# Performance work log

Hardware: AMD Instinct MI355X
Metric: run time of the kernel (lower is better)

## Reference

```python
import jax, jax.numpy as jnp
import numpy as np

KH = KW = 3
PAD = 1
STRIDE = 1
C_IN = 32
C_OUT = 16
H = W = 64
B = 64
H_OUT = (H - KH + 2 * PAD) // STRIDE + 1
W_OUT = (W - KW + 2 * PAD) // STRIDE + 1
S = H_OUT * W_OUT
K = C_IN * KH * KW


def unfold_2d(x):
    # x: [B, C, H, W] -> [B, C*KH*KW, S], torch.nn.functional.unfold ordering
    xp = jnp.pad(x, ((0, 0), (0, 0), (PAD, PAD), (PAD, PAD)))
    patches = []
    for i in range(KH):
        for j in range(KW):
            patches.append(xp[:, :, i:i + H_OUT * STRIDE:STRIDE, j:j + W_OUT * STRIDE:STRIDE])
    u = jnp.stack(patches, axis=2)  # [B, C, KH*KW, H_OUT, W_OUT]
    return u.reshape(x.shape[0], K, S)


def setup_inputs() -> dict:
    key = jax.random.key(0)
    k1, k2, k3 = jax.random.split(key, 3)
    X = jax.random.normal(k1, (B, C_IN, H, W), dtype=jnp.float32)
    # kaiming normal (linear): std = 1/sqrt(fan_in), fan_in = K for each location's GEMM
    weight = jax.random.normal(k2, (S, K, C_OUT), dtype=jnp.float32) / jnp.sqrt(jnp.float32(K))
    # xavier uniform over [H_OUT, W_OUT]
    lim = np.sqrt(6.0 / (H_OUT + W_OUT))
    bias = jax.random.uniform(k3, (H_OUT, W_OUT), dtype=jnp.float32, minval=-lim, maxval=lim)
    return {"X": X, "weight": weight, "bias": bias}


def reference(X, weight, bias):
    ufld = unfold_2d(X)                               # [B, K, S]
    ufld = ufld + bias.reshape(1, 1, -1)              # bias added per-location to patches
    h = jnp.einsum('bks,skc->bcs', ufld, weight)      # per-location unshared GEMM
    return h.reshape(X.shape[0], C_OUT, H_OUT, W_OUT)
```

## Files before the change

### kernel.cpp

```cpp
#include <hip/hip_runtime.h>
#include <stdint.h>
#include <stddef.h>

#define HOUT 64
#define WOUT 64
#define CIN  32
#define COUT 16
#define BATCH 64
#define SLOC 4096
#define KTOT 288
#define HPAD 66

typedef __attribute__((ext_vector_type(8))) short  short8;
typedef __attribute__((ext_vector_type(4))) float  floatx4;

static __device__ __forceinline__ unsigned short f2bf(float f) {
    union { float f; unsigned int u; } v; v.f = f;
    unsigned int u = v.u;
    unsigned int r = (u + 0x7FFFu + ((u >> 16) & 1u)) >> 16;
    return (unsigned short)r;
}

__global__ __launch_bounds__(256, 4) void prep_kernel(const float* __restrict__ X,
                                                      const float* __restrict__ Wg,
                                                      const float* __restrict__ bias,
                                                      unsigned short* __restrict__ xt,
                                                      uint4* __restrict__ wt,
                                                      float* __restrict__ bsum) {
    const int id   = blockIdx.x;
    const int tid  = threadIdx.x;
    const int lane = tid & 63;
    const int wv   = tid >> 6;

    if (id < 260) {
        int h1, w1;
        if (id < 66)       { h1 = 0;  w1 = id; }
        else if (id < 132) { h1 = 65; w1 = id - 66; }
        else { int r = id - 132; h1 = (r >> 1) + 1; w1 = (r & 1) ? 65 : 0; }
        ((uint4*)(xt + (size_t)(h1 * HPAD + w1) * 2048))[tid] = uint4{0u, 0u, 0u, 0u};
    }

    {
        const int w   = tid >> 2;
        const int cg8 = (tid & 3) * 8;
#pragma unroll
        for (int u = 0; u < 4; ++u) {
            const int unit = id * 4 + u;
            const int h = unit >> 6, b = unit & 63;
            const float* xb = X + (((size_t)b * CIN + cg8) * HOUT + h) * WOUT + w;
            unsigned short v[8];
#pragma unroll
            for (int j = 0; j < 8; ++j)
                v[j] = f2bf(xb[(size_t)j * HOUT * WOUT]);
            uint4 pack;
            pack.x = (unsigned)v[0] | ((unsigned)v[1] << 16);
            pack.y = (unsigned)v[2] | ((unsigned)v[3] << 16);
            pack.z = (unsigned)v[4] | ((unsigned)v[5] << 16);
            pack.w = (unsigned)v[6] | ((unsigned)v[7] << 16);
            *(uint4*)(xt + (size_t)((h + 1) * HPAD + (w + 1)) * 2048 + b * CIN + cg8) = pack;
        }
    }

    {
        const int lo = id & 7;
        const int q4 = (id >> 3) & 3;
        const int g  = ((id >> 5) << 3) | lo;
        const int s  = g * 16 + q4 * 4 + wv;
        const int q = lane >> 4, n = lane & 15;

        const float* wb = Wg + (size_t)s * (KTOT * COUT) + (size_t)(8 * q) * 9 * COUT + n;
        float csum = 0.f;
#pragma unroll
        for (int t = 0; t < 9; ++t) {
            float w[8];
#pragma unroll
            for (int j = 0; j < 8; ++j)
                w[j] = wb[(size_t)t * COUT + (size_t)j * 9 * COUT];
            unsigned short hh[8];
#pragma unroll
            for (int j = 0; j < 8; ++j) { csum += w[j]; hh[j] = f2bf(w[j]); }
            uint4 pack;
            pack.x = (unsigned)hh[0] | ((unsigned)hh[1] << 16);
            pack.y = (unsigned)hh[2] | ((unsigned)hh[3] << 16);
            pack.z = (unsigned)hh[4] | ((unsigned)hh[5] << 16);
            pack.w = (unsigned)hh[6] | ((unsigned)hh[7] << 16);
            wt[(size_t)(s * 9 + t) * 64 + lane] = pack;
        }
        csum += __shfl_xor(csum, 16, 64);
        csum += __shfl_xor(csum, 32, 64);
        if (lane < 16) bsum[s * COUT + n] = bias[s] * csum;
    }
}

__global__ __launch_bounds__(256, 4) void varconv_kernel(const unsigned short* __restrict__ xt,
                                                         const uint4* __restrict__ wt,
                                                         const float* __restrict__ bsum,
                                                         float* __restrict__ out) {
    __shared__ float lds[16 * 324];

    int id = blockIdx.x;
    int lo = id & 7;
    int q4 = (id >> 3) & 3;
    int g  = ((id >> 5) << 3) | lo;
    int s0 = g * 16;
    int y  = s0 >> 6;
    int x0 = s0 & 63;
    int B0 = q4 * 16;

    int lane = threadIdx.x & 63, wv = threadIdx.x >> 6;
    int q = lane >> 4;
    int n = lane & 15;

#pragma unroll
    for (int i = 0; i < 4; ++i) {
        int sl = wv * 4 + i;
        int s  = s0 + sl;
        int x  = x0 + sl;

        const uint4* wf = wt + (size_t)s * 9 * 64 + lane;
        short8 bf[9];
#pragma unroll
        for (int t = 0; t < 9; ++t)
            bf[t] = *(const short8*)(wf + t * 64);

        float badd = bsum[s * COUT + n];

        const unsigned short* ab = xt + (size_t)(B0 + n) * CIN + q * 8;
        short8 af[9];
#pragma unroll
        for (int t = 0; t < 9; ++t) {
            const int cy = t / 3, cx = t % 3;
            af[t] = *(const short8*)(ab + (size_t)((y + cy) * HPAD + (x + cx)) * 2048);
        }

        floatx4 acc = {0.f, 0.f, 0.f, 0.f};
#pragma unroll
        for (int t = 0; t < 9; ++t)
            acc = __builtin_amdgcn_mfma_f32_16x16x32_bf16(af[t], bf[t], acc, 0, 0, 0);

        int slot = q ^ (n & 3);
        floatx4 v = {acc[0] + badd, acc[1] + badd, acc[2] + badd, acc[3] + badd};
        *(floatx4*)&lds[n * 324 + sl * 20 + slot * 4] = v;
    }

    __syncthreads();

    int c   = lane >> 2;
    int slg = lane & 3;
#pragma unroll
    for (int i2 = 0; i2 < 4; ++i2) {
        int ib   = wv * 4 + i2;
        int slot = (ib >> 2) ^ (c & 3);
        float o0[4];
#pragma unroll
        for (int e = 0; e < 4; ++e)
            o0[e] = lds[c * 324 + (slg * 4 + e) * 20 + slot * 4 + (ib & 3)];
        floatx4 o = {o0[0], o0[1], o0[2], o0[3]};
        *(floatx4*)(out + ((size_t)((B0 + ib) * COUT + c)) * SLOC + s0 + slg * 4) = o;
    }
}

extern "C" void kernel_launch(void* const* d_in, const int* in_sizes, int n_in,
                              void* d_out, int out_size, void* d_ws, size_t ws_size,
                              hipStream_t stream) {
    const float* X    = (const float*)d_in[0];
    const float* Wg   = (const float*)d_in[1];
    const float* bias = (const float*)d_in[2];
    float* out = (float*)d_out;

    unsigned short* xt = (unsigned short*)d_ws;
    uint4* wt   = (uint4*)((char*)d_ws + 17842176);
    float* bsum = (float*)((char*)d_ws + 17842176 + 37748736);

    prep_kernel<<<1024, 256, 0, stream>>>(X, Wg, bias, xt, wt, bsum);
    varconv_kernel<<<1024, 256, 0, stream>>>(xt, wt, bsum, out);
}
```

Baseline: 166.0 us.

## Fuse weight bf16 conversion and bias-sum into conv kernel, drop workspace round-trip

Weight conversion to bf16 and the per-location weight column sums used for the bias term now happen inside the conv kernel, read straight from the fp32 weights. This removes writing and re-reading a ~38MB bf16 weight buffer and the bsum buffer through global memory. The prep kernel now only transposes X, split over twice as many blocks with half the work each. The trade-off is that the conv kernel does strided fp32 weight loads and extra conversion work per wave, which can raise register pressure.

```diff
diff --git a/kernel.cpp b/kernel.cpp
--- a/kernel.cpp
+++ b/kernel.cpp
@@ -21,16 +21,10 @@
     return (unsigned short)r;
 }
 
-__global__ __launch_bounds__(256, 4) void prep_kernel(const float* __restrict__ X,
-                                                      const float* __restrict__ Wg,
-                                                      const float* __restrict__ bias,
-                                                      unsigned short* __restrict__ xt,
-                                                      uint4* __restrict__ wt,
-                                                      float* __restrict__ bsum) {
-    const int id   = blockIdx.x;
-    const int tid  = threadIdx.x;
-    const int lane = tid & 63;
-    const int wv   = tid >> 6;
+__global__ __launch_bounds__(256) void prep_kernel(const float* __restrict__ X,
+                                                   unsigned short* __restrict__ xt) {
+    const int id  = blockIdx.x;
+    const int tid = threadIdx.x;
 
     if (id < 260) {
         int h1, w1;
@@ -40,61 +34,29 @@
         ((uint4*)(xt + (size_t)(h1 * HPAD + w1) * 2048))[tid] = uint4{0u, 0u, 0u, 0u};
     }
 
-    {
-        const int w   = tid >> 2;
-        const int cg8 = (tid & 3) * 8;
+    const int w   = tid >> 2;
+    const int cg8 = (tid & 3) * 8;
 #pragma unroll
-        for (int u = 0; u < 4; ++u) {
-            const int unit = id * 4 + u;
-            const int h = unit >> 6, b = unit & 63;
-            const float* xb = X + (((size_t)b * CIN + cg8) * HOUT + h) * WOUT + w;
-            unsigned short v[8];
+    for (int u = 0; u < 2; ++u) {
+        const int unit = id * 2 + u;
+        const int h = unit >> 6, b = unit & 63;
+        const float* xb = X + (((size_t)b * CIN + cg8) * HOUT + h) * WOUT + w;
+        unsigned short v[8];
 #pragma unroll
-            for (int j = 0; j < 8; ++j)
-                v[j] = f2bf(xb[(size_t)j * HOUT * WOUT]);
-            uint4 pack;
-            pack.x = (unsigned)v[0] | ((unsigned)v[1] << 16);
-            pack.y = (unsigned)v[2] | ((unsigned)v[3] << 16);
-            pack.z = (unsigned)v[4] | ((unsigned)v[5] << 16);
-            pack.w = (unsigned)v[6] | ((unsigned)v[7] << 16);
-            *(uint4*)(xt + (size_t)((h + 1) * HPAD + (w + 1)) * 2048 + b * CIN + cg8) = pack;
-        }
-    }
-
-    {
-        const int lo = id & 7;
-        const int q4 = (id >> 3) & 3;
-        const int g  = ((id >> 5) << 3) | lo;
-        const int s  = g * 16 + q4 * 4 + wv;
-        const int q = lane >> 4, n = lane & 15;
-
-        const float* wb = Wg + (size_t)s * (KTOT * COUT) + (size_t)(8 * q) * 9 * COUT + n;
-        float csum = 0.f;
-#pragma unroll
-        for (int t = 0; t < 9; ++t) {
-            float w[8];
-#pragma unroll
-            for (int j = 0; j < 8; ++j)
-                w[j] = wb[(size_t)t * COUT + (size_t)j * 9 * COUT];
-            unsigned short hh[8];
-#pragma unroll
-            for (int j = 0; j < 8; ++j) { csum += w[j]; hh[j] = f2bf(w[j]); }
-            uint4 pack;
-            pack.x = (unsigned)hh[0] | ((unsigned)hh[1] << 16);
-            pack.y = (unsigned)hh[2] | ((unsigned)hh[3] << 16);
-            pack.z = (unsigned)hh[4] | ((unsigned)hh[5] << 16);
-            pack.w = (unsigned)hh[6] | ((unsigned)hh[7] << 16);
-            wt[(size_t)(s * 9 + t) * 64 + lane] = pack;
-        }
-        csum += __shfl_xor(csum, 16, 64);
-        csum += __shfl_xor(csum, 32, 64);
-        if (lane < 16) bsum[s * COUT + n] = bias[s] * csum;
+        for (int j = 0; j < 8; ++j)
+            v[j] = f2bf(xb[(size_t)j * HOUT * WOUT]);
+        uint4 pack;
+        pack.x = (unsigned)v[0] | ((unsigned)v[1] << 16);
+        pack.y = (unsigned)v[2] | ((unsigned)v[3] << 16);
+        pack.z = (unsigned)v[4] | ((unsigned)v[5] << 16);
+        pack.w = (unsigned)v[6] | ((unsigned)v[7] << 16);
+        *(uint4*)(xt + (size_t)((h + 1) * HPAD + (w + 1)) * 2048 + b * CIN + cg8) = pack;
     }
 }
 
 __global__ __launch_bounds__(256, 4) void varconv_kernel(const unsigned short* __restrict__ xt,
-                                                         const uint4* __restrict__ wt,
-                                                         const float* __restrict__ bsum,
+                                                         const float* __restrict__ Wg,
+                                                         const float* __restrict__ bias,
                                                          float* __restrict__ out) {
     __shared__ float lds[16 * 324];
 
@@ -117,14 +79,6 @@
         int s  = s0 + sl;
         int x  = x0 + sl;
 
-        const uint4* wf = wt + (size_t)s * 9 * 64 + lane;
-        short8 bf[9];
-#pragma unroll
-        for (int t = 0; t < 9; ++t)
-            bf[t] = *(const short8*)(wf + t * 64);
-
-        float badd = bsum[s * COUT + n];
-
         const unsigned short* ab = xt + (size_t)(B0 + n) * CIN + q * 8;
         short8 af[9];
 #pragma unroll
@@ -132,6 +86,35 @@
             const int cy = t / 3, cx = t % 3;
             af[t] = *(const short8*)(ab + (size_t)((y + cy) * HPAD + (x + cx)) * 2048);
         }
+
+        const float* wb = Wg + (size_t)s * (KTOT * COUT) + n;
+        float csum = 0.f;
+        short8 bf[9];
+#pragma unroll
+        for (int tg = 0; tg < 3; ++tg) {
+            float wreg[3][8];
+#pragma unroll
+            for (int tt = 0; tt < 3; ++tt)
+#pragma unroll
+                for (int j = 0; j < 8; ++j)
+                    wreg[tt][j] = wb[(size_t)((8 * q + j) * 9 + (tg * 3 + tt)) * COUT];
+#pragma unroll
+            for (int tt = 0; tt < 3; ++tt) {
+                unsigned short hh[8];
+#pragma unroll
+                for (int j = 0; j < 8; ++j) { csum += wreg[tt][j]; hh[j] = f2bf(wreg[tt][j]); }
+                union { uint4 u; short8 s8; } cv;
+                cv.u.x = (unsigned)hh[0] | ((unsigned)hh[1] << 16);
+                cv.u.y = (unsigned)hh[2] | ((unsigned)hh[3] << 16);
+                cv.u.z = (unsigned)hh[4] | ((unsigned)hh[5] << 16);
+                cv.u.w = (unsigned)hh[6] | ((unsigned)hh[7] << 16);
+                bf[tg * 3 + tt] = cv.s8;
+            }
+        }
+
+        csum += __shfl_xor(csum, 16, 64);
+        csum += __shfl_xor(csum, 32, 64);
+        float badd = bias[s] * csum;
 
         floatx4 acc = {0.f, 0.f, 0.f, 0.f};
 #pragma unroll
@@ -169,9 +152,7 @@
     float* out = (float*)d_out;
 
     unsigned short* xt = (unsigned short*)d_ws;
-    uint4* wt   = (uint4*)((char*)d_ws + 17842176);
-    float* bsum = (float*)((char*)d_ws + 17842176 + 37748736);
 
-    prep_kernel<<<1024, 256, 0, stream>>>(X, Wg, bias, xt, wt, bsum);
-    varconv_kernel<<<1024, 256, 0, stream>>>(xt, wt, bsum, out);
+    prep_kernel<<<2048, 256, 0, stream>>>(X, xt);
+    varconv_kernel<<<1024, 256, 0, stream>>>(xt, Wg, bias, out);
 }
```

New measurement: 181.7 us. +9.4%, slower.
